# Kernel tuning notes

Measured on AMD Instinct MI355X. Metric: run time of the kernel, lower is better.

Reference implementation:

```python
import jax, jax.numpy as jnp
from jax import lax
import numpy as np

B, L, D = 2, 2048, 768
DI, DS, DTR, K = 1536, 16, 48, 4  # d_inner, d_state, dt_rank, d_conv
EPS = 1e-5


def layernorm(x, g, b):
    mu = jnp.mean(x, axis=-1, keepdims=True)
    var = jnp.mean(jnp.square(x - mu), axis=-1, keepdims=True)
    return (x - mu) * lax.rsqrt(var + EPS) * g + b


def mamba(x, in_w, conv_w, conv_b, xproj_w, dt_w, dt_b, A_log, Dp, out_w):
    # x: [B, L, D]
    xz = x @ in_w.T                       # [B, L, 2*DI]
    xc, z = jnp.split(xz, 2, axis=-1)     # [B, L, DI] each
    # causal depthwise conv1d, kernel K, left pad K-1, truncate to L
    xp = jnp.pad(xc, ((0, 0), (K - 1, 0), (0, 0)))
    conv = conv_b + sum(xp[:, k:k + L, :] * conv_w[:, k] for k in range(K))
    xc = jax.nn.silu(conv)
    dbc = xc @ xproj_w.T                  # [B, L, DTR+2*DS]
    dt = dbc[..., :DTR]
    Bm = dbc[..., DTR:DTR + DS]           # [B, L, DS]
    Cm = dbc[..., DTR + DS:]              # [B, L, DS]
    dt = jax.nn.softplus(dt @ dt_w.T + dt_b)  # [B, L, DI]
    A = -jnp.exp(A_log)                   # [DI, DS]

    def step(h, inp):
        dt_t, B_t, C_t, x_t = inp         # [B,DI], [B,DS], [B,DS], [B,DI]
        dA = jnp.exp(dt_t[..., None] * A)               # [B, DI, DS]
        h = dA * h + (dt_t * x_t)[..., None] * B_t[:, None, :]
        y = jnp.einsum('bds,bs->bd', h, C_t)
        return h, y

    h0 = jnp.zeros((x.shape[0], DI, DS), x.dtype)
    _, ys = lax.scan(step, h0, (dt.transpose(1, 0, 2), Bm.transpose(1, 0, 2),
                                Cm.transpose(1, 0, 2), xc.transpose(1, 0, 2)))
    y = ys.transpose(1, 0, 2) + xc * Dp   # [B, L, DI]
    y = y * jax.nn.silu(z)
    return y @ out_w.T                    # [B, L, D]


def setup_inputs() -> dict:
    key = jax.random.key(0)
    ks = iter(jax.random.split(key, 40))
    r = lambda s, sc=0.02: jax.random.normal(next(ks), s, jnp.float32) * sc
    A0 = jnp.log(jnp.broadcast_to(jnp.arange(1, DS + 1, dtype=jnp.float32), (DI, DS)))
    def mamba_params(p):
        return {
            f'{p}_in_w': r((2 * DI, D)), f'{p}_conv_w': r((DI, K), 0.2),
            f'{p}_conv_b': jnp.zeros((DI,)), f'{p}_xproj_w': r((DTR + 2 * DS, DI)),
            f'{p}_dt_w': r((DI, DTR), 0.1), f'{p}_dt_b': jnp.zeros((DI,)),
            f'{p}_A_log': A0, f'{p}_D': jnp.ones((DI,)), f'{p}_out_w': r((D, DI)),
        }
    inp = {'x': jax.random.normal(next(ks), (B, L, D), jnp.float32),
           'norm_g': jnp.ones((D,)), 'norm_b': jnp.zeros((D,))}
    inp.update(mamba_params('f'))
    inp.update(mamba_params('b'))
    inp.update({'mix_w': r((D, 2 * D)), 'mix_b': jnp.zeros((D,)),
                'ffn_w1': r((4 * D, D)), 'ffn_b1': jnp.zeros((4 * D,)),
                'ffn_w2': r((D, 4 * D)), 'ffn_b2': jnp.zeros((D,)),
                'ffn_norm_g': jnp.ones((D,)), 'ffn_norm_b': jnp.zeros((D,))})
    return inp


def reference(x, norm_g, norm_b,
              f_in_w, f_conv_w, f_conv_b, f_xproj_w, f_dt_w, f_dt_b, f_A_log, f_D, f_out_w,
              b_in_w, b_conv_w, b_conv_b, b_xproj_w, b_dt_w, b_dt_b, b_A_log, b_D, b_out_w,
              mix_w, mix_b, ffn_w1, ffn_b1, ffn_w2, ffn_b2, ffn_norm_g, ffn_norm_b):
    residual = x
    xn = layernorm(x, norm_g, norm_b)
    xf = mamba(xn, f_in_w, f_conv_w, f_conv_b, f_xproj_w, f_dt_w, f_dt_b, f_A_log, f_D, f_out_w)
    xb = mamba(jnp.flip(xn, axis=1), b_in_w, b_conv_w, b_conv_b, b_xproj_w,
               b_dt_w, b_dt_b, b_A_log, b_D, b_out_w)
    xb = jnp.flip(xb, axis=1)
    xm = jnp.concatenate([xf, xb], axis=-1) @ mix_w.T + mix_b
    h = xm + residual
    hn = layernorm(h, ffn_norm_g, ffn_norm_b)
    ff = jax.nn.gelu(hn @ ffn_w1.T + ffn_b1) @ ffn_w2.T + ffn_b2  # dropout = eval identity
    return ff + h
```

## Files before the change

kernel.cpp:

```cpp
#include <hip/hip_runtime.h>
#include <hip/hip_bf16.h>
#include <math.h>

#define NB 2
#define LL 2048
#define DD 768
#define DI 1536
#define DS 16
#define MM (NB*LL)
#define TCH 64
#define NCH 32

typedef __hip_bfloat16 bf16;
typedef __attribute__((ext_vector_type(8))) __bf16 bf16x8;
typedef __attribute__((ext_vector_type(4))) float f32x4;

__device__ __forceinline__ float b2f(bf16 v){ return __bfloat162float(v); }
__device__ __forceinline__ bf16 f2b(float v){ return __float2bfloat16(v); }

__device__ __forceinline__ void un2(unsigned u, float& lo, float& hi){
  union {unsigned i; float f;} a, b;
  a.i = u << 16; b.i = u & 0xffff0000u;
  lo = a.f; hi = b.f;
}

__device__ __forceinline__ void async_cp16(const bf16* g, __bf16* l) {
  __builtin_amdgcn_global_load_lds((const __attribute__((address_space(1))) void*)g,
                                   (__attribute__((address_space(3))) void*)l, 16, 0, 0);
}

#define ACT_NONE 0
#define ACT_SOFTPLUS 1
#define ACT_GELU 2

__device__ __forceinline__ float apply_act(float v, int act) {
  if (act == ACT_SOFTPLUS) {
    v = (v > 15.f) ? v : log1pf(__expf(v));
  } else if (act == ACT_GELU) {
    float u = 0.7978845608028654f * (v + 0.044715f*v*v*v);
    v = 0.5f * v * (1.f + tanhf(u));
  }
  return v;
}

__global__ void gemm_kernel(const bf16* __restrict__ A, int lda,
                            const bf16* __restrict__ B, int ldb,
                            void* __restrict__ C, int ldc,
                            int N, int K,
                            const float* __restrict__ bias,
                            const float* __restrict__ addp, int ldadd,
                            int act, int f32out)
{
  __shared__ __bf16 As[128*64];
  __shared__ __bf16 Bs[128*64];
  const int tid  = threadIdx.x;
  const int lane = tid & 63, wave = tid >> 6;
  const int m0 = blockIdx.x * 128, n0 = blockIdx.y * 128;
  const int wm = wave & 1, wn = wave >> 1;

  const int srow = wave*32 + (lane >> 3);
  const int gsw  = (lane & 7) ^ ((lane >> 3) & 7);
  const int scol = gsw * 8;
  const bf16* Ag[4]; const bf16* Bg[4];
  __bf16 *AsW[4], *BsW[4];
  #pragma unroll
  for (int i = 0; i < 4; i++) {
    int ar = m0 + srow + i*8;
    Ag[i] = A + (size_t)ar * lda + scol;
    int br = n0 + srow + i*8; if (br > N-1) br = N-1;
    Bg[i] = B + (size_t)br * ldb + scol;
    AsW[i] = &As[(wave*32 + i*8)*64];
    BsW[i] = &Bs[(wave*32 + i*8)*64];
  }

  f32x4 acc[4][4] = {};
  const int arow = wm*64 + (lane & 15);
  const int brow = wn*64 + (lane & 15);
  const int rx = lane & 7;
  const int gq = lane >> 4;

  for (int kb = 0; kb < K; kb += 64) {
    __syncthreads();
    #pragma unroll
    for (int i = 0; i < 4; i++) {
      async_cp16(Ag[i] + kb, AsW[i]);
      async_cp16(Bg[i] + kb, BsW[i]);
    }
    __syncthreads();
    #pragma unroll
    for (int h = 0; h < 2; h++) {
      const int kk = ((h*4 + gq) ^ rx) * 8;
      bf16x8 af[4], bfr[4];
      #pragma unroll
      for (int i = 0; i < 4; i++) af[i]  = *(const bf16x8*)&As[(arow + i*16)*64 + kk];
      #pragma unroll
      for (int j = 0; j < 4; j++) bfr[j] = *(const bf16x8*)&Bs[(brow + j*16)*64 + kk];
      #pragma unroll
      for (int i = 0; i < 4; i++)
        #pragma unroll
        for (int j = 0; j < 4; j++)
          acc[i][j] = __builtin_amdgcn_mfma_f32_16x16x32_bf16(af[i], bfr[j], acc[i][j], 0, 0, 0);
    }
  }

  bf16*  Cb = (bf16*)C;
  float* Cf = (float*)C;
  #pragma unroll
  for (int i = 0; i < 4; i++) {
    int rbase = m0 + wm*64 + i*16 + (lane >> 4)*4;
    #pragma unroll
    for (int j = 0; j < 4; j++) {
      int col = n0 + wn*64 + j*16 + (lane & 15);
      if (col >= N) continue;
      float bv = bias ? bias[col] : 0.f;
      #pragma unroll
      for (int r = 0; r < 4; r++) {
        int row = rbase + r;
        float v = apply_act(acc[i][j][r] + bv, act);
        if (addp) v += addp[(size_t)row * ldadd + col];
        if (f32out) Cf[(size_t)row * ldc + col] = v;
        else        Cb[(size_t)row * ldc + col] = f2b(v);
      }
    }
  }
}

__global__ void gemm64_kernel(const bf16* __restrict__ A, int lda, size_t sA,
                              const bf16* __restrict__ B, int ldb, size_t sB,
                              void* __restrict__ C, int ldc, size_t sC,
                              int N, int K,
                              const float* __restrict__ bias0,
                              const float* __restrict__ bias1, int biasBase,
                              const float* __restrict__ addp, int ldadd,
                              int act, int f32out)
{
  __shared__ __bf16 As[64*64];
  __shared__ __bf16 Bs[64*64];
  const int tid  = threadIdx.x;
  const int lane = tid & 63, wave = tid >> 6;
  const int z = blockIdx.z;
  A += (size_t)z * sA;
  B += (size_t)z * sB;
  const float* bias = ((biasBase + z) ? bias1 : bias0);
  const int m0 = blockIdx.x * 64, n0 = blockIdx.y * 64;
  const int wm = wave & 1, wn = wave >> 1;

  const int srow = wave*16 + (lane >> 3);
  const int gsw  = (lane & 7) ^ ((lane >> 3) & 7);
  const int scol = gsw * 8;
  const bf16* Ag[2]; const bf16* Bg[2];
  __bf16 *AsW[2], *BsW[2];
  #pragma unroll
  for (int i = 0; i < 2; i++) {
    int ar = m0 + srow + i*8;
    Ag[i] = A + (size_t)ar * lda + scol;
    int br = n0 + srow + i*8; if (br > N-1) br = N-1;
    Bg[i] = B + (size_t)br * ldb + scol;
    AsW[i] = &As[(wave*16 + i*8)*64];
    BsW[i] = &Bs[(wave*16 + i*8)*64];
  }

  f32x4 acc[2][2] = {};
  const int arow = wm*32 + (lane & 15);
  const int brow = wn*32 + (lane & 15);
  const int rx = lane & 7;
  const int gq = lane >> 4;

  for (int kb = 0; kb < K; kb += 64) {
    __syncthreads();
    #pragma unroll
    for (int i = 0; i < 2; i++) {
      async_cp16(Ag[i] + kb, AsW[i]);
      async_cp16(Bg[i] + kb, BsW[i]);
    }
    __syncthreads();
    #pragma unroll
    for (int h = 0; h < 2; h++) {
      const int kk = ((h*4 + gq) ^ rx) * 8;
      bf16x8 af[2], bfr[2];
      #pragma unroll
      for (int i = 0; i < 2; i++) af[i]  = *(const bf16x8*)&As[(arow + i*16)*64 + kk];
      #pragma unroll
      for (int j = 0; j < 2; j++) bfr[j] = *(const bf16x8*)&Bs[(brow + j*16)*64 + kk];
      #pragma unroll
      for (int i = 0; i < 2; i++)
        #pragma unroll
        for (int j = 0; j < 2; j++)
          acc[i][j] = __builtin_amdgcn_mfma_f32_16x16x32_bf16(af[i], bfr[j], acc[i][j], 0, 0, 0);
    }
  }

  bf16*  Cb = (bf16*)C + z*sC;
  float* Cf = (float*)C + z*sC;
  #pragma unroll
  for (int i = 0; i < 2; i++) {
    int rbase = m0 + wm*32 + i*16 + (lane >> 4)*4;
    #pragma unroll
    for (int j = 0; j < 2; j++) {
      int col = n0 + wn*32 + j*16 + (lane & 15);
      if (col >= N) continue;
      float bv = bias ? bias[col] : 0.f;
      #pragma unroll
      for (int r = 0; r < 4; r++) {
        int row = rbase + r;
        float v = apply_act(acc[i][j][r] + bv, act);
        if (addp) v += addp[(size_t)row * ldadd + col];
        if (f32out) Cf[(size_t)row * ldc + col] = v;
        else        Cb[(size_t)row * ldc + col] = f2b(v);
      }
    }
  }
}

__global__ void ln_kernel(const float* __restrict__ x, const float* __restrict__ g,
                          const float* __restrict__ b, bf16* __restrict__ out)
{
  const int row = blockIdx.x;
  const int tid = threadIdx.x;
  const float* xr = x + (size_t)row * DD;
  float v[3], s = 0.f, s2 = 0.f;
  #pragma unroll
  for (int i = 0; i < 3; i++) {
    float f = xr[tid + i*256];
    v[i] = f; s += f; s2 += f*f;
  }
  #pragma unroll
  for (int o = 32; o > 0; o >>= 1) { s += __shfl_down(s, o, 64); s2 += __shfl_down(s2, o, 64); }
  __shared__ float ps[4], ps2[4];
  int wave = tid >> 6;
  if ((tid & 63) == 0) { ps[wave] = s; ps2[wave] = s2; }
  __syncthreads();
  s = ps[0]+ps[1]+ps[2]+ps[3]; s2 = ps2[0]+ps2[1]+ps2[2]+ps2[3];
  float mu = s * (1.f/DD);
  float var = s2 * (1.f/DD) - mu*mu;
  float rs = rsqrtf(var + 1e-5f);
  #pragma unroll
  for (int i = 0; i < 3; i++) {
    int c = tid + i*256;
    float o = (v[i] - mu) * rs * g[c] + b[c];
    out[(size_t)row * DD + c] = f2b(o);
  }
}

__global__ void conv_silu_kernel(const bf16* __restrict__ xz, int ldxz, int xzDirOff,
                                 const float* __restrict__ cw0, const float* __restrict__ cb0,
                                 const float* __restrict__ cw1, const float* __restrict__ cb1,
                                 bf16* __restrict__ xc, size_t sXc, int dirBase)
{
  int idx = blockIdx.x * 256 + threadIdx.x;
  int sIdx = (idx >= DI) ? 1 : 0;
  int d = idx - sIdx*DI;
  int dir = dirBase + sIdx;
  int row = blockIdx.y;
  int b = row >> 11, t = row & 2047;
  const float* cw = dir ? cw1 : cw0;
  const float* cb = dir ? cb1 : cb0;
  float acc = cb[d];
  float w0 = cw[d*4+0], w1 = cw[d*4+1], w2 = cw[d*4+2], w3 = cw[d*4+3];
  const bf16* base = xz + (size_t)(b*2048) * ldxz + sIdx*xzDirOff + d;
  if (dir == 0) {
    if (t >= 3) acc += b2f(base[(size_t)(t-3)*ldxz]) * w0;
    if (t >= 2) acc += b2f(base[(size_t)(t-2)*ldxz]) * w1;
    if (t >= 1) acc += b2f(base[(size_t)(t-1)*ldxz]) * w2;
    acc += b2f(base[(size_t)t*ldxz]) * w3;
  } else {
    if (t <= 2044) acc += b2f(base[(size_t)(t+3)*ldxz]) * w0;
    if (t <= 2045) acc += b2f(base[(size_t)(t+2)*ldxz]) * w1;
    if (t <= 2046) acc += b2f(base[(size_t)(t+1)*ldxz]) * w2;
    acc += b2f(base[(size_t)t*ldxz]) * w3;
  }
  float y = acc / (1.f + __expf(-acc));
  xc[sIdx*sXc + (size_t)row * DI + d] = f2b(y);
}

#define SZ_INW (2*DI*DD)
#define SZ_XP  (80*DI)
#define SZ_OUT (DD*DI)
#define SZ_DTW (DI*64)
#define SZ_AN  (DI*16)
#define SZ_MIX (2*DD*DD)
#define SZ_F1  (4*DD*DD)
__global__ void prep_all_kernel(const float* fi, const float* bi,
                                const float* fxp, const float* bxp,
                                const float* fo, const float* bo,
                                const float* fdt, const float* bdt,
                                const float* fa, const float* ba,
                                const float* mw, const float* f1, const float* f2,
                                bf16* w_in, bf16* w_xp2, bf16* w_out2, bf16* dtwp2,
                                float* An2, bf16* w_mix, bf16* w_f1, bf16* w_f2)
{
  int i = blockIdx.x * 256 + threadIdx.x;
  if (i < SZ_INW) { w_in[i] = f2b(fi[i]); return; }               i -= SZ_INW;
  if (i < SZ_INW) { w_in[SZ_INW + i] = f2b(bi[i]); return; }      i -= SZ_INW;
  if (i < SZ_XP)  { w_xp2[i] = f2b(fxp[i]); return; }             i -= SZ_XP;
  if (i < SZ_XP)  { w_xp2[SZ_XP + i] = f2b(bxp[i]); return; }     i -= SZ_XP;
  if (i < SZ_OUT) { w_out2[i] = f2b(fo[i]); return; }             i -= SZ_OUT;
  if (i < SZ_OUT) { w_out2[SZ_OUT + i] = f2b(bo[i]); return; }    i -= SZ_OUT;
  if (i < SZ_DTW) { int r=i>>6,c=i&63; dtwp2[i] = (c<48)?f2b(fdt[r*48+c]):f2b(0.f); return; } i -= SZ_DTW;
  if (i < SZ_DTW) { int r=i>>6,c=i&63; dtwp2[SZ_DTW+i] = (c<48)?f2b(bdt[r*48+c]):f2b(0.f); return; } i -= SZ_DTW;
  if (i < SZ_AN)  { int d=i>>4,s=i&15; An2[s*DI+d] = -__expf(fa[i]); return; } i -= SZ_AN;
  if (i < SZ_AN)  { int d=i>>4,s=i&15; An2[SZ_AN + s*DI+d] = -__expf(ba[i]); return; } i -= SZ_AN;
  if (i < SZ_MIX) { w_mix[i] = f2b(mw[i]); return; }              i -= SZ_MIX;
  if (i < SZ_F1)  { w_f1[i] = f2b(f1[i]); return; }               i -= SZ_F1;
  w_f2[i] = f2b(f2[i]);
}

__global__ void scan_partial(const bf16* __restrict__ dt, size_t sDt,
                             const bf16* __restrict__ xc, size_t sXc,
                             const bf16* __restrict__ dbc, size_t sDbc,
                             const float* __restrict__ An, size_t sAn,
                             float* __restrict__ Pp, float* __restrict__ Sp,
                             int dirBase)
{
  const int tid = threadIdx.x;
  const int sIdx = blockIdx.z >> 1, b = blockIdx.z & 1;
  const int dir = dirBase + sIdx;
  const int c = blockIdx.y;
  const int d = blockIdx.x * 256 + tid;
  dt  += sIdx*sDt; xc += sIdx*sXc; dbc += sIdx*sDbc;
  const int rowbase = b*2048 + c*TCH;
  __shared__ unsigned bcs[TCH*16];
  for (int i = tid; i < TCH*16; i += 256) {
    int r = i >> 4, dw = i & 15;
    bcs[i] = ((const unsigned*)(dbc + (size_t)(rowbase + r)*96 + 48))[dw];
  }
  __syncthreads();
  float A[16], P[16], g[16];
  #pragma unroll
  for (int s = 0; s < 16; s++) { A[s] = An[sIdx*sAn + s*DI + d]; P[s] = 1.f; g[s] = 0.f; }
  int ph0 = dir ? (TCH-1) : 0;
  float dtv = b2f(dt[(size_t)(rowbase+ph0)*DI + d]);
  float xv  = b2f(xc[(size_t)(rowbase+ph0)*DI + d]);
  for (int t = 0; t < TCH; t++) {
    const int ph = dir ? (TCH-1-t) : t;
    const int tn = (t+1 < TCH) ? t+1 : t;
    const int phn = dir ? (TCH-1-tn) : tn;
    float dtn = b2f(dt[(size_t)(rowbase+phn)*DI + d]);
    float xvn = b2f(xc[(size_t)(rowbase+phn)*DI + d]);
    unsigned ub[8];
    *(uint4*)&ub[0] = *(const uint4*)&bcs[ph*16];
    *(uint4*)&ub[4] = *(const uint4*)&bcs[ph*16 + 4];
    float Bv[16];
    #pragma unroll
    for (int k = 0; k < 8; k++) un2(ub[k], Bv[2*k], Bv[2*k+1]);
    float u = dtv * xv;
    #pragma unroll
    for (int s = 0; s < 16; s++) {
      float dA = __expf(dtv * A[s]);
      P[s] *= dA;
      g[s] = dA * g[s] + u * Bv[s];
    }
    dtv = dtn; xv = xvn;
  }
  size_t base = ((((size_t)sIdx*NB + b)*NCH + c)*DI + d) * 16;
  #pragma unroll
  for (int s = 0; s < 16; s++) { Pp[base+s] = P[s]; Sp[base+s] = g[s]; }
}

__global__ void scan_combine(const float* __restrict__ Pp, const float* __restrict__ Sp,
                             float* __restrict__ h0, int dirBase)
{
  const int j = blockIdx.x * 256 + threadIdx.x;
  const int b = blockIdx.y;
  const int sIdx = blockIdx.z;
  const int dir = dirBase + sIdx;
  float h = 0.f;
  for (int k = 0; k < NCH; k++) {
    int c = dir ? (NCH-1-k) : k;
    size_t idx = (((size_t)sIdx*NB + b)*NCH + c)*DI*16 + j;
    h0[idx] = h;
    h = Pp[idx]*h + Sp[idx];
  }
}

__global__ void scan_final(const bf16* __restrict__ dt, size_t sDt,
                           const bf16* __restrict__ xc, size_t sXc,
                           const bf16* __restrict__ dbc, size_t sDbc,
                           const bf16* __restrict__ xz, int ldxz, int xzDirOff,
                           const float* __restrict__ An, size_t sAn,
                           const float* __restrict__ Dp0, const float* __restrict__ Dp1,
                           const float* __restrict__ h0,
                           bf16* __restrict__ yout, size_t sY, int dirBase)
{
  const int tid = threadIdx.x;
  const int sIdx = blockIdx.z >> 1, b = blockIdx.z & 1;
  const int dir = dirBase + sIdx;
  const int c = blockIdx.y;
  const int d = blockIdx.x * 256 + tid;
  dt += sIdx*sDt; xc += sIdx*sXc; dbc += sIdx*sDbc; yout += sIdx*sY;
  const float* Dp = dir ? Dp1 : Dp0;
  const int rowbase = b*2048 + c*TCH;
  __shared__ unsigned bcs[TCH*16];
  for (int i = tid; i < TCH*16; i += 256) {
    int r = i >> 4, dw = i & 15;
    bcs[i] = ((const unsigned*)(dbc + (size_t)(rowbase + r)*96 + 48))[dw];
  }
  __syncthreads();
  float A[16], h[16];
  size_t hbase = ((((size_t)sIdx*NB + b)*NCH + c)*DI + d) * 16;
  #pragma unroll
  for (int s = 0; s < 16; s++) { A[s] = An[sIdx*sAn + s*DI + d]; h[s] = h0[hbase+s]; }
  const float Dd = Dp[d];
  const bf16* zp = xz + sIdx*xzDirOff + DI + d;
  int ph0 = dir ? (TCH-1) : 0;
  float dtv = b2f(dt[(size_t)(rowbase+ph0)*DI + d]);
  float xv  = b2f(xc[(size_t)(rowbase+ph0)*DI + d]);
  float zv  = b2f(zp[(size_t)(rowbase+ph0)*ldxz]);
  for (int t = 0; t < TCH; t++) {
    const int ph = dir ? (TCH-1-t) : t;
    const int row = rowbase + ph;
    const int tn = (t+1 < TCH) ? t+1 : t;
    const int phn = dir ? (TCH-1-tn) : tn;
    float dtn = b2f(dt[(size_t)(rowbase+phn)*DI + d]);
    float xvn = b2f(xc[(size_t)(rowbase+phn)*DI + d]);
    float zvn = b2f(zp[(size_t)(rowbase+phn)*ldxz]);
    unsigned ub[8], uc[8];
    *(uint4*)&ub[0] = *(const uint4*)&bcs[ph*16];
    *(uint4*)&ub[4] = *(const uint4*)&bcs[ph*16 + 4];
    *(uint4*)&uc[0] = *(const uint4*)&bcs[ph*16 + 8];
    *(uint4*)&uc[4] = *(const uint4*)&bcs[ph*16 + 12];
    float Bv[16], Cv[16];
    #pragma unroll
    for (int k = 0; k < 8; k++) { un2(ub[k], Bv[2*k], Bv[2*k+1]); un2(uc[k], Cv[2*k], Cv[2*k+1]); }
    float u = dtv * xv;
    float y = 0.f;
    #pragma unroll
    for (int s = 0; s < 16; s++) {
      float dA = __expf(dtv * A[s]);
      h[s] = dA * h[s] + u * Bv[s];
      y += h[s] * Cv[s];
    }
    float yg = (y + xv * Dd) * (zv / (1.f + __expf(-zv)));
    yout[(size_t)row*DI + d] = f2b(yg);
    dtv = dtn; xv = xvn; zv = zvn;
  }
}

extern "C" void kernel_launch(void* const* d_in, const int* in_sizes, int n_in,
                              void* d_out, int out_size, void* d_ws, size_t ws_size,
                              hipStream_t stream)
{
  const float* x      = (const float*)d_in[0];
  const float* norm_g = (const float*)d_in[1];
  const float* norm_b = (const float*)d_in[2];
  const float* fi  = (const float*)d_in[3];
  const float* fcw = (const float*)d_in[4];
  const float* fcb = (const float*)d_in[5];
  const float* fxp = (const float*)d_in[6];
  const float* fdt = (const float*)d_in[7];
  const float* fdb = (const float*)d_in[8];
  const float* fa  = (const float*)d_in[9];
  const float* fD  = (const float*)d_in[10];
  const float* fo  = (const float*)d_in[11];
  const float* bi  = (const float*)d_in[12];
  const float* bcw = (const float*)d_in[13];
  const float* bcb = (const float*)d_in[14];
  const float* bxp = (const float*)d_in[15];
  const float* bdt = (const float*)d_in[16];
  const float* bdb = (const float*)d_in[17];
  const float* ba  = (const float*)d_in[18];
  const float* bD  = (const float*)d_in[19];
  const float* bo  = (const float*)d_in[20];
  const float* mix_w  = (const float*)d_in[21];
  const float* mix_b  = (const float*)d_in[22];
  const float* ffn_w1 = (const float*)d_in[23];
  const float* ffn_b1 = (const float*)d_in[24];
  const float* ffn_w2 = (const float*)d_in[25];
  const float* ffn_b2 = (const float*)d_in[26];
  const float* ffn_ng = (const float*)d_in[27];
  const float* ffn_nb = (const float*)d_in[28];

  auto al = [](size_t x){ return (x + 255) & ~(size_t)255; };
  const size_t fixedB =
      al((size_t)2*SZ_AN*4) + al((size_t)2*SZ_DTW*2) + al((size_t)2*SZ_INW*2) +
      al((size_t)2*SZ_XP*2) + al((size_t)2*SZ_OUT*2) + al((size_t)SZ_MIX*2) +
      al((size_t)SZ_F1*2) + al((size_t)SZ_F1*2) + al((size_t)MM*DD*2) + al((size_t)MM*DI*2);
  const size_t concB = fixedB + al((size_t)MM*2*DI*2*2) + 2*al((size_t)2*MM*DI*2) +
      al((size_t)2*MM*96*2) + 3*al((size_t)2*NB*NCH*DI*16*4);
  const bool conc = (ws_size >= concB);

  size_t o = 0;
  char* wsb = (char*)d_ws;
  auto nxt = [&](size_t bytes) -> char* {
    char* p = wsb + o; o += (bytes + 255) & ~(size_t)255; return p;
  };
  float* An2   = (float*)nxt((size_t)2*SZ_AN*4);
  bf16*  dtwp2 = (bf16*) nxt((size_t)2*SZ_DTW*2);
  bf16*  w_in  = (bf16*) nxt((size_t)2*SZ_INW*2);
  bf16*  w_xp2 = (bf16*) nxt((size_t)2*SZ_XP*2);
  bf16*  w_out2= (bf16*) nxt((size_t)2*SZ_OUT*2);
  bf16*  w_mix = (bf16*) nxt((size_t)SZ_MIX*2);
  bf16*  w_f1  = (bf16*) nxt((size_t)SZ_F1*2);
  bf16*  w_f2  = (bf16*) nxt((size_t)SZ_F1*2);
  bf16*  xn    = (bf16*) nxt((size_t)MM*DD*2);
  bf16*  xfb   = (bf16*) nxt((size_t)MM*DI*2);

  bf16 *xz, *xc, *dtb, *dbc;  float *Pp, *Sp, *h0, *hbuf;
  int ldxz, xzDirOff;
  size_t sXc, sDbc, sDt;
  if (conc) {
    xz  = (bf16*) nxt((size_t)MM*2*DI*2*2);
    xc  = (bf16*) nxt((size_t)2*MM*DI*2);
    dtb = (bf16*) nxt((size_t)2*MM*DI*2);
    dbc = (bf16*) nxt((size_t)2*MM*96*2);
    Pp  = (float*)nxt((size_t)2*NB*NCH*DI*16*4);
    Sp  = (float*)nxt((size_t)2*NB*NCH*DI*16*4);
    h0  = (float*)nxt((size_t)2*NB*NCH*DI*16*4);
    hbuf = Pp;
    ldxz = 2*2*DI; xzDirOff = 2*DI;
    sXc = (size_t)MM*DI; sDbc = (size_t)MM*96; sDt = (size_t)MM*DI;
  } else {
    xz  = (bf16*) nxt((size_t)MM*2*DI*2);
    xc  = (bf16*) nxt((size_t)MM*DI*2);
    dtb = (bf16*) nxt((size_t)MM*DI*2);
    dbc = (bf16*) nxt((size_t)MM*96*2);
    Pp  = (float*)nxt((size_t)NB*NCH*DI*16*4);
    Sp  = (float*)nxt((size_t)NB*NCH*DI*16*4);
    h0  = (float*)nxt((size_t)NB*NCH*DI*16*4);
    hbuf = (float*)dtb;
    ldxz = 2*DI; xzDirOff = 0;
    sXc = 0; sDbc = 0; sDt = 0;
  }
  bf16* hn = xn;
  bf16* a1 = xz;

  const int prepN = 2*SZ_INW + 2*SZ_XP + 2*SZ_OUT + 2*SZ_DTW + 2*SZ_AN + SZ_MIX + 2*SZ_F1;
  prep_all_kernel<<<(prepN + 255)/256, 256, 0, stream>>>(
      fi, bi, fxp, bxp, fo, bo, fdt, bdt, fa, ba, mix_w, ffn_w1, ffn_w2,
      w_in, w_xp2, w_out2, dtwp2, An2, w_mix, w_f1, w_f2);

  ln_kernel<<<MM, 256, 0, stream>>>(x, norm_g, norm_b, xn);

  if (conc) {
    gemm_kernel<<<dim3(32, 48), 256, 0, stream>>>(xn, DD, w_in, DD, xz, ldxz,
                                                  2*2*DI, DD, nullptr, nullptr, 0,
                                                  ACT_NONE, 0);
    conv_silu_kernel<<<dim3(12, MM), 256, 0, stream>>>(xz, ldxz, xzDirOff,
                                                       fcw, fcb, bcw, bcb, xc, sXc, 0);
    gemm64_kernel<<<dim3(64, 2, 2), 256, 0, stream>>>(xc, DI, sXc, w_xp2, DI, (size_t)SZ_XP,
                                                      dbc, 96, sDbc, 80, DI,
                                                      nullptr, nullptr, 0, nullptr, 0, ACT_NONE, 0);
    gemm64_kernel<<<dim3(64, 24, 2), 256, 0, stream>>>(dbc, 96, sDbc, dtwp2, 64, (size_t)SZ_DTW,
                                                       dtb, DI, sDt, DI, 64,
                                                       fdb, bdb, 0, nullptr, 0, ACT_SOFTPLUS, 0);
    scan_partial<<<dim3(DI/256, NCH, 4), 256, 0, stream>>>(dtb, sDt, xc, sXc, dbc, sDbc,
                                                           An2, (size_t)SZ_AN, Pp, Sp, 0);
    scan_combine<<<dim3(DI*16/256, NB, 2), 256, 0, stream>>>(Pp, Sp, h0, 0);
    scan_final<<<dim3(DI/256, NCH, 4), 256, 0, stream>>>(dtb, sDt, xc, sXc, dbc, sDbc,
                                                         xz, ldxz, xzDirOff, An2, (size_t)SZ_AN,
                                                         fD, bD, h0, xc, sXc, 0);
    gemm64_kernel<<<dim3(64, 12, 2), 256, 0, stream>>>(xc, DI, sXc, w_out2, DI, (size_t)SZ_OUT,
                                                       xfb, 2*DD, (size_t)DD, DD, DI,
                                                       nullptr, nullptr, 0, nullptr, 0, ACT_NONE, 0);
  } else {
    for (int dir = 0; dir < 2; ++dir) {
      gemm_kernel<<<dim3(32, 24), 256, 0, stream>>>(xn, DD, w_in + (size_t)dir*SZ_INW, DD,
                                                    xz, ldxz, 2*DI, DD, nullptr, nullptr, 0,
                                                    ACT_NONE, 0);
      conv_silu_kernel<<<dim3(6, MM), 256, 0, stream>>>(xz, ldxz, 0,
                                                        fcw, fcb, bcw, bcb, xc, 0, dir);
      gemm64_kernel<<<dim3(64, 2, 1), 256, 0, stream>>>(xc, DI, 0, w_xp2 + (size_t)dir*SZ_XP, DI, 0,
                                                        dbc, 96, 0, 80, DI,
                                                        nullptr, nullptr, 0, nullptr, 0, ACT_NONE, 0);
      gemm64_kernel<<<dim3(64, 24, 1), 256, 0, stream>>>(dbc, 96, 0, dtwp2 + (size_t)dir*SZ_DTW, 64, 0,
                                                         dtb, DI, 0, DI, 64,
                                                         fdb, bdb, dir, nullptr, 0, ACT_SOFTPLUS, 0);
      scan_partial<<<dim3(DI/256, NCH, 2), 256, 0, stream>>>(dtb, 0, xc, 0, dbc, 0,
                                                             An2 + (size_t)dir*SZ_AN, 0, Pp, Sp, dir);
      scan_combine<<<dim3(DI*16/256, NB, 1), 256, 0, stream>>>(Pp, Sp, h0, dir);
      scan_final<<<dim3(DI/256, NCH, 2), 256, 0, stream>>>(dtb, 0, xc, 0, dbc, 0,
                                                           xz, ldxz, 0, An2 + (size_t)dir*SZ_AN, 0,
                                                           fD, bD, h0, xc, 0, dir);
      gemm64_kernel<<<dim3(64, 12, 1), 256, 0, stream>>>(xc, DI, 0, w_out2 + (size_t)dir*SZ_OUT, DI, 0,
                                                         (void*)((bf16*)xfb + dir*DD), 2*DD, 0, DD, DI,
                                                         nullptr, nullptr, 0, nullptr, 0, ACT_NONE, 0);
    }
  }

  gemm64_kernel<<<dim3(64, 12, 1), 256, 0, stream>>>(xfb, 2*DD, 0, w_mix, 2*DD, 0,
                                                     hbuf, DD, 0, DD, 2*DD,
                                                     mix_b, mix_b, 0, x, DD, ACT_NONE, 1);
  ln_kernel<<<MM, 256, 0, stream>>>(hbuf, ffn_ng, ffn_nb, hn);
  gemm_kernel<<<dim3(32, 24), 256, 0, stream>>>(hn, DD, w_f1, DD, a1, 4*DD,
                                                4*DD, DD, ffn_b1, nullptr, 0, ACT_GELU, 0);
  gemm64_kernel<<<dim3(64, 12, 1), 256, 0, stream>>>(a1, 4*DD, 0, w_f2, 4*DD, 0,
                                                     d_out, DD, 0, DD, 4*DD,
                                                     ffn_b2, ffn_b2, 0, hbuf, DD, ACT_NONE, 1);
}
```

Baseline: 633.5 us.

## Add 256x256 multi-stage async GEMM and retile projection GEMMs

Adds a 512-thread GEMM with 256x256 tiles, a 4-deep async global-to-LDS pipeline using 128KB of dynamic LDS, swizzled LDS layout and raised wave priority around the MFMA loop. It is used for the in-projection and FFN-up GEMMs. The out-projection, mix and FFN-down GEMMs move from the 64-tile kernel to the 128-tile kernel, which gains batch strides. The aim is more data reuse per tile and better overlap of loads with MFMA work. The trade-off is fewer blocks than CUs for several GEMMs, so load imbalance and low occupancy are possible.

New measurement: 777.3 us. +22.7%, slower.

```diff
diff --git a/kernel.cpp b/kernel.cpp
--- a/kernel.cpp
+++ b/kernel.cpp
@@ -43,9 +43,99 @@
   return v;
 }
 
-__global__ void gemm_kernel(const bf16* __restrict__ A, int lda,
-                            const bf16* __restrict__ B, int ldb,
-                            void* __restrict__ C, int ldc,
+__global__ __launch_bounds__(512, 2)
+void gemm256_kernel(const bf16* __restrict__ A, int lda,
+                    const bf16* __restrict__ B, int ldb,
+                    bf16* __restrict__ C, int ldc, int K,
+                    const float* __restrict__ bias, int act)
+{
+  extern __shared__ __bf16 lds[];
+  __bf16* As = lds;
+  __bf16* Bs = lds + 32768;
+  const int tid  = threadIdx.x;
+  const int lane = tid & 63, wave = tid >> 6;
+  const int m0 = blockIdx.x * 256, n0 = blockIdx.y * 256;
+  const int wm = wave >> 2, wn = wave & 3;
+  const int f = lane & 15, gq = lane >> 4;
+
+  const int sl = lane >> 2, spg = lane & 3;
+  const bf16* AgS[2]; const bf16* BgS[2];
+  int dst[2];
+  #pragma unroll
+  for (int i = 0; i < 2; i++) {
+    int lr = wave*32 + i*16 + sl;
+    int lg = spg ^ (lr & 3) ^ ((lr >> 2) & 3);
+    AgS[i] = A + (size_t)(m0 + lr) * lda + lg*8;
+    BgS[i] = B + (size_t)(n0 + lr) * ldb + lg*8;
+    dst[i] = (wave*32 + i*16) * 32;
+  }
+  const int swz = (f & 3) ^ ((f >> 2) & 3);
+  const int pg8 = (gq ^ swz) * 8;
+  int aoff[8], boff[4];
+  #pragma unroll
+  for (int i = 0; i < 8; i++) aoff[i] = (wm*128 + i*16 + f)*32 + pg8;
+  #pragma unroll
+  for (int j = 0; j < 4; j++) boff[j] = (wn*64 + j*16 + f)*32 + pg8;
+
+  const int NT = K >> 5;
+#define STAGE256(tt) { \
+    const int kb_ = (tt) * 32; const int bo_ = ((tt) & 3) * 8192; \
+    async_cp16(AgS[0] + kb_, As + bo_ + dst[0]); \
+    async_cp16(AgS[1] + kb_, As + bo_ + dst[1]); \
+    async_cp16(BgS[0] + kb_, Bs + bo_ + dst[0]); \
+    async_cp16(BgS[1] + kb_, Bs + bo_ + dst[1]); }
+
+  STAGE256(0);
+  if (NT > 1) STAGE256(1);
+  if (NT > 2) STAGE256(2);
+
+  f32x4 acc[8][4] = {};
+  for (int t = 0; t < NT; ++t) {
+    asm volatile("s_waitcnt lgkmcnt(0)" ::: "memory");
+    const int ahead = NT - 1 - t;
+    if (ahead > 1)       asm volatile("s_waitcnt vmcnt(8)" ::: "memory");
+    else if (ahead == 1) asm volatile("s_waitcnt vmcnt(4)" ::: "memory");
+    else                 asm volatile("s_waitcnt vmcnt(0)" ::: "memory");
+    __builtin_amdgcn_sched_barrier(0);
+    __builtin_amdgcn_s_barrier();
+    __builtin_amdgcn_sched_barrier(0);
+    if (t + 3 < NT) STAGE256(t+3);
+    const __bf16* Ab = As + (t & 3) * 8192;
+    const __bf16* Bb = Bs + (t & 3) * 8192;
+    bf16x8 af[8], bfr[4];
+    #pragma unroll
+    for (int j = 0; j < 4; j++) bfr[j] = *(const bf16x8*)&Bb[boff[j]];
+    #pragma unroll
+    for (int i = 0; i < 8; i++) af[i] = *(const bf16x8*)&Ab[aoff[i]];
+    __builtin_amdgcn_s_setprio(1);
+    #pragma unroll
+    for (int i = 0; i < 8; i++)
+      #pragma unroll
+      for (int j = 0; j < 4; j++)
+        acc[i][j] = __builtin_amdgcn_mfma_f32_16x16x32_bf16(af[i], bfr[j], acc[i][j], 0, 0, 0);
+    __builtin_amdgcn_s_setprio(0);
+  }
+#undef STAGE256
+
+  #pragma unroll
+  for (int i = 0; i < 8; i++) {
+    const int rbase = m0 + wm*128 + i*16 + gq*4;
+    #pragma unroll
+    for (int j = 0; j < 4; j++) {
+      const int col = n0 + wn*64 + j*16 + f;
+      const float bv = bias ? bias[col] : 0.f;
+      #pragma unroll
+      for (int r = 0; r < 4; r++) {
+        float v = apply_act(acc[i][j][r] + bv, act);
+        C[(size_t)(rbase + r) * ldc + col] = f2b(v);
+      }
+    }
+  }
+}
+
+__global__ void gemm_kernel(const bf16* __restrict__ A, int lda, size_t sA,
+                            const bf16* __restrict__ B, int ldb, size_t sB,
+                            void* __restrict__ C, int ldc, size_t sC,
                             int N, int K,
                             const float* __restrict__ bias,
                             const float* __restrict__ addp, int ldadd,
@@ -55,6 +145,9 @@
   __shared__ __bf16 Bs[128*64];
   const int tid  = threadIdx.x;
   const int lane = tid & 63, wave = tid >> 6;
+  const int z = blockIdx.z;
+  A += (size_t)z * sA;
+  B += (size_t)z * sB;
   const int m0 = blockIdx.x * 128, n0 = blockIdx.y * 128;
   const int wm = wave & 1, wn = wave >> 1;
 
@@ -103,8 +196,8 @@
     }
   }
 
-  bf16*  Cb = (bf16*)C;
-  float* Cf = (float*)C;
+  bf16*  Cb = (bf16*)C + (size_t)z * sC;
+  float* Cf = (float*)C + (size_t)z * sC;
   #pragma unroll
   for (int i = 0; i < 4; i++) {
     int rbase = m0 + wm*64 + i*16 + (lane >> 4)*4;
@@ -470,6 +563,13 @@
   const float* ffn_ng = (const float*)d_in[27];
   const float* ffn_nb = (const float*)d_in[28];
 
+  static int s_attr = 0;
+  if (!s_attr) {
+    hipFuncSetAttribute((const void*)gemm256_kernel,
+                        hipFuncAttributeMaxDynamicSharedMemorySize, 131072);
+    s_attr = 1;
+  }
+
   auto al = [](size_t x){ return (x + 255) & ~(size_t)255; };
   const size_t fixedB =
       al((size_t)2*SZ_AN*4) + al((size_t)2*SZ_DTW*2) + al((size_t)2*SZ_INW*2) +
@@ -532,9 +632,8 @@
   ln_kernel<<<MM, 256, 0, stream>>>(x, norm_g, norm_b, xn);
 
   if (conc) {
-    gemm_kernel<<<dim3(32, 48), 256, 0, stream>>>(xn, DD, w_in, DD, xz, ldxz,
-                                                  2*2*DI, DD, nullptr, nullptr, 0,
-                                                  ACT_NONE, 0);
+    gemm256_kernel<<<dim3(16, 24), 512, 131072, stream>>>(xn, DD, w_in, DD,
+                                                          xz, ldxz, DD, nullptr, ACT_NONE);
     conv_silu_kernel<<<dim3(12, MM), 256, 0, stream>>>(xz, ldxz, xzDirOff,
                                                        fcw, fcb, bcw, bcb, xc, sXc, 0);
     gemm64_kernel<<<dim3(64, 2, 2), 256, 0, stream>>>(xc, DI, sXc, w_xp2, DI, (size_t)SZ_XP,
@@ -549,14 +648,13 @@
     scan_final<<<dim3(DI/256, NCH, 4), 256, 0, stream>>>(dtb, sDt, xc, sXc, dbc, sDbc,
                                                          xz, ldxz, xzDirOff, An2, (size_t)SZ_AN,
                                                          fD, bD, h0, xc, sXc, 0);
-    gemm64_kernel<<<dim3(64, 12, 2), 256, 0, stream>>>(xc, DI, sXc, w_out2, DI, (size_t)SZ_OUT,
-                                                       xfb, 2*DD, (size_t)DD, DD, DI,
-                                                       nullptr, nullptr, 0, nullptr, 0, ACT_NONE, 0);
+    gemm_kernel<<<dim3(32, 6, 2), 256, 0, stream>>>(xc, DI, sXc, w_out2, DI, (size_t)SZ_OUT,
+                                                    xfb, 2*DD, (size_t)DD, DD, DI,
+                                                    nullptr, nullptr, 0, ACT_NONE, 0);
   } else {
     for (int dir = 0; dir < 2; ++dir) {
-      gemm_kernel<<<dim3(32, 24), 256, 0, stream>>>(xn, DD, w_in + (size_t)dir*SZ_INW, DD,
-                                                    xz, ldxz, 2*DI, DD, nullptr, nullptr, 0,
-                                                    ACT_NONE, 0);
+      gemm256_kernel<<<dim3(16, 12), 512, 131072, stream>>>(xn, DD, w_in + (size_t)dir*SZ_INW, DD,
+                                                            xz, ldxz, DD, nullptr, ACT_NONE);
       conv_silu_kernel<<<dim3(6, MM), 256, 0, stream>>>(xz, ldxz, 0,
                                                         fcw, fcb, bcw, bcb, xc, 0, dir);
       gemm64_kernel<<<dim3(64, 2, 1), 256, 0, stream>>>(xc, DI, 0, w_xp2 + (size_t)dir*SZ_XP, DI, 0,
@@ -571,19 +669,19 @@
       scan_final<<<dim3(DI/256, NCH, 2), 256, 0, stream>>>(dtb, 0, xc, 0, dbc, 0,
                                                            xz, ldxz, 0, An2 + (size_t)dir*SZ_AN, 0,
                                                            fD, bD, h0, xc, 0, dir);
-      gemm64_kernel<<<dim3(64, 12, 1), 256, 0, stream>>>(xc, DI, 0, w_out2 + (size_t)dir*SZ_OUT, DI, 0,
-                                                         (void*)((bf16*)xfb + dir*DD), 2*DD, 0, DD, DI,
-                                                         nullptr, nullptr, 0, nullptr, 0, ACT_NONE, 0);
-    }
-  }
-
-  gemm64_kernel<<<dim3(64, 12, 1), 256, 0, stream>>>(xfb, 2*DD, 0, w_mix, 2*DD, 0,
-                                                     hbuf, DD, 0, DD, 2*DD,
-                                                     mix_b, mix_b, 0, x, DD, ACT_NONE, 1);
+      gemm_kernel<<<dim3(32, 6, 1), 256, 0, stream>>>(xc, DI, 0, w_out2 + (size_t)dir*SZ_OUT, DI, 0,
+                                                      (void*)((bf16*)xfb + dir*DD), 2*DD, 0, DD, DI,
+                                                      nullptr, nullptr, 0, ACT_NONE, 0);
+    }
+  }
+
+  gemm_kernel<<<dim3(32, 6, 1), 256, 0, stream>>>(xfb, 2*DD, 0, w_mix, 2*DD, 0,
+                                                  hbuf, DD, 0, DD, 2*DD,
+                                                  mix_b, x, DD, ACT_NONE, 1);
   ln_kernel<<<MM, 256, 0, stream>>>(hbuf, ffn_ng, ffn_nb, hn);
-  gemm_kernel<<<dim3(32, 24), 256, 0, stream>>>(hn, DD, w_f1, DD, a1, 4*DD,
-                                                4*DD, DD, ffn_b1, nullptr, 0, ACT_GELU, 0);
-  gemm64_kernel<<<dim3(64, 12, 1), 256, 0, stream>>>(a1, 4*DD, 0, w_f2, 4*DD, 0,
-                                                     d_out, DD, 0, DD, 4*DD,
-                                                     ffn_b2, ffn_b2, 0, hbuf, DD, ACT_NONE, 1);
-}
+  gemm256_kernel<<<dim3(16, 12), 512, 131072, stream>>>(hn, DD, w_f1, DD,
+                                                        a1, 4*DD, DD, ffn_b1, ACT_GELU);
+  gemm_kernel<<<dim3(32, 6, 1), 256, 0, stream>>>(a1, 4*DD, 0, w_f2, 4*DD, 0,
+                                                  d_out, DD, 0, DD, 4*DD,
+                                                  ffn_b2, hbuf, DD, ACT_NONE, 1);
+}
```

## Replace 128x128 GEMM with 256x256 double-buffered 8-wave ping-pong GEMM

Applied to the files above, without the earlier changes.

Replaces the single-buffered 128x128 tile GEMM with a 512-thread kernel that computes 256x256 output tiles. It uses 128KB of dynamic LDS split into double buffers, and issues async global-to-LDS copies interleaved with MFMA quarters, with explicit barriers, s_setprio and vmcnt waits. The aim is to overlap global loads with matrix math and raise data reuse per tile for the in-projection and FFN-up GEMMs. It drops the N-bounds clamping and the residual-add/f32 output paths, so it relies on N and K being multiples of 256 and 128. The larger tile also gives fewer blocks: 384 for the in-projection and 192 for FFN-up.

Measured after the change: 677.3 us. 6.9% more time.

```diff
diff --git a/kernel.cpp b/kernel.cpp
--- a/kernel.cpp
+++ b/kernel.cpp
@@ -43,86 +43,123 @@
   return v;
 }
 
-__global__ void gemm_kernel(const bf16* __restrict__ A, int lda,
-                            const bf16* __restrict__ B, int ldb,
-                            void* __restrict__ C, int ldc,
-                            int N, int K,
-                            const float* __restrict__ bias,
-                            const float* __restrict__ addp, int ldadd,
-                            int act, int f32out)
-{
-  __shared__ __bf16 As[128*64];
-  __shared__ __bf16 Bs[128*64];
+__global__ __launch_bounds__(512, 2)
+void gemm8p_kernel(const bf16* __restrict__ A, int lda,
+                   const bf16* __restrict__ B, int ldb,
+                   bf16* __restrict__ C, int ldc, int K,
+                   const float* __restrict__ bias, int act)
+{
+  extern __shared__ __bf16 lds[];
+  __bf16* As = lds;
+  __bf16* Bs = lds + 32768;
   const int tid  = threadIdx.x;
   const int lane = tid & 63, wave = tid >> 6;
-  const int m0 = blockIdx.x * 128, n0 = blockIdx.y * 128;
-  const int wm = wave & 1, wn = wave >> 1;
-
-  const int srow = wave*32 + (lane >> 3);
-  const int gsw  = (lane & 7) ^ ((lane >> 3) & 7);
-  const int scol = gsw * 8;
-  const bf16* Ag[4]; const bf16* Bg[4];
-  __bf16 *AsW[4], *BsW[4];
-  #pragma unroll
-  for (int i = 0; i < 4; i++) {
-    int ar = m0 + srow + i*8;
-    Ag[i] = A + (size_t)ar * lda + scol;
-    int br = n0 + srow + i*8; if (br > N-1) br = N-1;
-    Bg[i] = B + (size_t)br * ldb + scol;
-    AsW[i] = &As[(wave*32 + i*8)*64];
-    BsW[i] = &Bs[(wave*32 + i*8)*64];
-  }
-
-  f32x4 acc[4][4] = {};
-  const int arow = wm*64 + (lane & 15);
-  const int brow = wn*64 + (lane & 15);
-  const int rx = lane & 7;
-  const int gq = lane >> 4;
-
-  for (int kb = 0; kb < K; kb += 64) {
-    __syncthreads();
+  const int m0 = blockIdx.x * 256, n0 = blockIdx.y * 256;
+  const int wm = wave >> 2, wn = wave & 3;
+  const int f = lane & 15, gq = lane >> 4, rx = lane & 7;
+
+  const int srow = wave*16 + (lane >> 3);
+  const int sgrp = (lane & 7) ^ ((lane >> 3) & 7);
+  const bf16* Ast = A + (size_t)(m0 + srow) * lda + sgrp*8;
+  const bf16* Bst = B + (size_t)(n0 + srow) * ldb + sgrp*8;
+  const size_t lda8 = (size_t)8*lda, ldb8 = (size_t)8*ldb;
+  const size_t lda128 = (size_t)128*lda, ldb128 = (size_t)128*ldb;
+  const int sdst = wave*16*64;
+
+#define STG_A(buf, half, kt) { \
+    async_cp16(Ast + (half)*lda128 + (kt)*64,        As + (buf)*16384 + (half)*8192 + sdst); \
+    async_cp16(Ast + (half)*lda128 + lda8 + (kt)*64, As + (buf)*16384 + (half)*8192 + sdst + 512); }
+#define STG_B(buf, half, kt) { \
+    async_cp16(Bst + (half)*ldb128 + (kt)*64,        Bs + (buf)*16384 + (half)*8192 + sdst); \
+    async_cp16(Bst + (half)*ldb128 + ldb8 + (kt)*64, Bs + (buf)*16384 + (half)*8192 + sdst + 512); }
+
+  const int kk0 = (gq ^ rx) * 8;
+  const int kk1 = ((4 + gq) ^ rx) * 8;
+  const int arow = (wm*128 + f) * 64;
+  const int brow = (wn*64  + f) * 64;
+  bf16x8 af[4][2], b0[2][2], b1[2][2];
+
+#define RD_A(buf, mq) { _Pragma("unroll") for (int i = 0; i < 4; i++) { \
+    const __bf16* p = &As[(buf)*16384 + arow + ((mq)*64 + i*16)*64]; \
+    af[i][0] = *(const bf16x8*)&p[kk0]; af[i][1] = *(const bf16x8*)&p[kk1]; } }
+#define RD_B(buf, nq, dst) { _Pragma("unroll") for (int j = 0; j < 2; j++) { \
+    const __bf16* p = &Bs[(buf)*16384 + brow + ((nq)*32 + j*16)*64]; \
+    dst[j][0] = *(const bf16x8*)&p[kk0]; dst[j][1] = *(const bf16x8*)&p[kk1]; } }
+#define MFQ(mq, nq, bset) { __builtin_amdgcn_s_setprio(1); \
+    _Pragma("unroll") for (int i = 0; i < 4; i++) \
+      _Pragma("unroll") for (int j = 0; j < 2; j++) { \
+        acc[(mq)*4+i][(nq)*2+j] = __builtin_amdgcn_mfma_f32_16x16x32_bf16(af[i][0], bset[j][0], acc[(mq)*4+i][(nq)*2+j], 0,0,0); \
+        acc[(mq)*4+i][(nq)*2+j] = __builtin_amdgcn_mfma_f32_16x16x32_bf16(af[i][1], bset[j][1], acc[(mq)*4+i][(nq)*2+j], 0,0,0); } \
+    __builtin_amdgcn_s_setprio(0); }
+#define SBAR { __builtin_amdgcn_sched_barrier(0); __builtin_amdgcn_s_barrier(); __builtin_amdgcn_sched_barrier(0); }
+
+  f32x4 acc[8][4] = {};
+  const int NT = K >> 6, NT2 = K >> 7;
+
+  STG_A(0,0,0); STG_A(0,1,0); STG_B(0,0,0); STG_B(0,1,0);
+  STG_B(1,0,1); STG_B(1,1,1);
+  asm volatile("s_waitcnt vmcnt(4)" ::: "memory");
+  SBAR;
+
+  for (int it = 0; it < NT2; ++it) {
+    const int te = 2*it, to = te + 1;
+    const bool more  = (te + 2 < NT);
+    const bool more3 = (to + 2 < NT);
+    const bool lastit = (it == NT2 - 1);
+    RD_A(0,0); RD_B(0,0,b0);
+    STG_A(1,0,to);
+    SBAR; MFQ(0,0,b0); SBAR;
+    RD_B(0,1,b1);
+    STG_A(1,1,to);
+    SBAR; MFQ(0,1,b1); SBAR;
+    RD_A(0,1);
+    if (more) STG_B(0,0,te+2);
+    SBAR; MFQ(1,0,b0); SBAR;
+    if (more) STG_B(0,1,te+2);
+    SBAR; MFQ(1,1,b1);
+    if (lastit) { asm volatile("s_waitcnt vmcnt(0)" ::: "memory"); }
+    else        { asm volatile("s_waitcnt vmcnt(4)" ::: "memory"); }
+    SBAR;
+    RD_A(1,0); RD_B(1,0,b0);
+    if (more) STG_A(0,0,te+2);
+    SBAR; MFQ(0,0,b0); SBAR;
+    RD_B(1,1,b1);
+    if (more) STG_A(0,1,te+2);
+    SBAR; MFQ(0,1,b1); SBAR;
+    RD_A(1,1);
+    if (more3) STG_B(1,0,to+2);
+    SBAR; MFQ(1,0,b0); SBAR;
+    if (more3) STG_B(1,1,to+2);
+    SBAR; MFQ(1,1,b1);
+    if (lastit) { asm volatile("s_waitcnt vmcnt(0)" ::: "memory"); }
+    else        { asm volatile("s_waitcnt vmcnt(4)" ::: "memory"); }
+    SBAR;
+  }
+#undef STG_A
+#undef STG_B
+#undef RD_A
+#undef RD_B
+#undef MFQ
+#undef SBAR
+
+  #pragma unroll
+  for (int mq = 0; mq < 2; mq++)
     #pragma unroll
     for (int i = 0; i < 4; i++) {
-      async_cp16(Ag[i] + kb, AsW[i]);
-      async_cp16(Bg[i] + kb, BsW[i]);
+      const int rbase = m0 + wm*128 + mq*64 + i*16 + gq*4;
+      #pragma unroll
+      for (int nq = 0; nq < 2; nq++)
+        #pragma unroll
+        for (int j = 0; j < 2; j++) {
+          const int col = n0 + wn*64 + nq*32 + j*16 + f;
+          const float bv = bias ? bias[col] : 0.f;
+          #pragma unroll
+          for (int r = 0; r < 4; r++) {
+            float v = apply_act(acc[mq*4+i][nq*2+j][r] + bv, act);
+            C[(size_t)(rbase + r) * ldc + col] = f2b(v);
+          }
+        }
     }
-    __syncthreads();
-    #pragma unroll
-    for (int h = 0; h < 2; h++) {
-      const int kk = ((h*4 + gq) ^ rx) * 8;
-      bf16x8 af[4], bfr[4];
-      #pragma unroll
-      for (int i = 0; i < 4; i++) af[i]  = *(const bf16x8*)&As[(arow + i*16)*64 + kk];
-      #pragma unroll
-      for (int j = 0; j < 4; j++) bfr[j] = *(const bf16x8*)&Bs[(brow + j*16)*64 + kk];
-      #pragma unroll
-      for (int i = 0; i < 4; i++)
-        #pragma unroll
-        for (int j = 0; j < 4; j++)
-          acc[i][j] = __builtin_amdgcn_mfma_f32_16x16x32_bf16(af[i], bfr[j], acc[i][j], 0, 0, 0);
-    }
-  }
-
-  bf16*  Cb = (bf16*)C;
-  float* Cf = (float*)C;
-  #pragma unroll
-  for (int i = 0; i < 4; i++) {
-    int rbase = m0 + wm*64 + i*16 + (lane >> 4)*4;
-    #pragma unroll
-    for (int j = 0; j < 4; j++) {
-      int col = n0 + wn*64 + j*16 + (lane & 15);
-      if (col >= N) continue;
-      float bv = bias ? bias[col] : 0.f;
-      #pragma unroll
-      for (int r = 0; r < 4; r++) {
-        int row = rbase + r;
-        float v = apply_act(acc[i][j][r] + bv, act);
-        if (addp) v += addp[(size_t)row * ldadd + col];
-        if (f32out) Cf[(size_t)row * ldc + col] = v;
-        else        Cb[(size_t)row * ldc + col] = f2b(v);
-      }
-    }
-  }
 }
 
 __global__ void gemm64_kernel(const bf16* __restrict__ A, int lda, size_t sA,
@@ -470,6 +507,13 @@
   const float* ffn_ng = (const float*)d_in[27];
   const float* ffn_nb = (const float*)d_in[28];
 
+  static int s_attr = 0;
+  if (!s_attr) {
+    hipFuncSetAttribute((const void*)gemm8p_kernel,
+                        hipFuncAttributeMaxDynamicSharedMemorySize, 131072);
+    s_attr = 1;
+  }
+
   auto al = [](size_t x){ return (x + 255) & ~(size_t)255; };
   const size_t fixedB =
       al((size_t)2*SZ_AN*4) + al((size_t)2*SZ_DTW*2) + al((size_t)2*SZ_INW*2) +
@@ -532,9 +576,8 @@
   ln_kernel<<<MM, 256, 0, stream>>>(x, norm_g, norm_b, xn);
 
   if (conc) {
-    gemm_kernel<<<dim3(32, 48), 256, 0, stream>>>(xn, DD, w_in, DD, xz, ldxz,
-                                                  2*2*DI, DD, nullptr, nullptr, 0,
-                                                  ACT_NONE, 0);
+    gemm8p_kernel<<<dim3(16, 24), 512, 131072, stream>>>(xn, DD, w_in, DD,
+                                                         xz, ldxz, DD, nullptr, ACT_NONE);
     conv_silu_kernel<<<dim3(12, MM), 256, 0, stream>>>(xz, ldxz, xzDirOff,
                                                        fcw, fcb, bcw, bcb, xc, sXc, 0);
     gemm64_kernel<<<dim3(64, 2, 2), 256, 0, stream>>>(xc, DI, sXc, w_xp2, DI, (size_t)SZ_XP,
@@ -554,9 +597,8 @@
                                                        nullptr, nullptr, 0, nullptr, 0, ACT_NONE, 0);
   } else {
     for (int dir = 0; dir < 2; ++dir) {
-      gemm_kernel<<<dim3(32, 24), 256, 0, stream>>>(xn, DD, w_in + (size_t)dir*SZ_INW, DD,
-                                                    xz, ldxz, 2*DI, DD, nullptr, nullptr, 0,
-                                                    ACT_NONE, 0);
+      gemm8p_kernel<<<dim3(16, 12), 512, 131072, stream>>>(xn, DD, w_in + (size_t)dir*SZ_INW, DD,
+                                                           xz, ldxz, DD, nullptr, ACT_NONE);
       conv_silu_kernel<<<dim3(6, MM), 256, 0, stream>>>(xz, ldxz, 0,
                                                         fcw, fcb, bcw, bcb, xc, 0, dir);
       gemm64_kernel<<<dim3(64, 2, 1), 256, 0, stream>>>(xc, DI, 0, w_xp2 + (size_t)dir*SZ_XP, DI, 0,
@@ -581,8 +623,8 @@
                                                      hbuf, DD, 0, DD, 2*DD,
                                                      mix_b, mix_b, 0, x, DD, ACT_NONE, 1);
   ln_kernel<<<MM, 256, 0, stream>>>(hbuf, ffn_ng, ffn_nb, hn);
-  gemm_kernel<<<dim3(32, 24), 256, 0, stream>>>(hn, DD, w_f1, DD, a1, 4*DD,
-                                                4*DD, DD, ffn_b1, nullptr, 0, ACT_GELU, 0);
+  gemm8p_kernel<<<dim3(16, 12), 512, 131072, stream>>>(hn, DD, w_f1, DD,
+                                                       a1, 4*DD, DD, ffn_b1, ACT_GELU);
   gemm64_kernel<<<dim3(64, 12, 1), 256, 0, stream>>>(a1, 4*DD, 0, w_f2, 4*DD, 0,
                                                      d_out, DD, 0, DD, 4*DD,
                                                      ffn_b2, ffn_b2, 0, hbuf, DD, ACT_NONE, 1);
```

## Double-buffer shared-memory tiles in both GEMM kernels to overlap loads with MFMA

Applied to the files above, without the earlier changes.

Both GEMM kernels now keep two LDS buffers for the A and B tiles. Each iteration issues the async copies for the next K-tile before running the MFMAs on the current one, and the loop uses one barrier per iteration instead of two. The aim is to hide global-to-LDS latency behind compute, at the cost of twice the LDS per block, which may lower occupancy. It relies on the async copies finishing before the barrier at the end of the iteration.

Measured after the change: 696.8 us. +10.0%, slower.

```diff
diff --git a/kernel.cpp b/kernel.cpp
--- a/kernel.cpp
+++ b/kernel.cpp
@@ -51,8 +51,8 @@
                             const float* __restrict__ addp, int ldadd,
                             int act, int f32out)
 {
-  __shared__ __bf16 As[128*64];
-  __shared__ __bf16 Bs[128*64];
+  __shared__ __bf16 As[2][128*64];
+  __shared__ __bf16 Bs[2][128*64];
   const int tid  = threadIdx.x;
   const int lane = tid & 63, wave = tid >> 6;
   const int m0 = blockIdx.x * 128, n0 = blockIdx.y * 128;
@@ -62,16 +62,19 @@
   const int gsw  = (lane & 7) ^ ((lane >> 3) & 7);
   const int scol = gsw * 8;
   const bf16* Ag[4]; const bf16* Bg[4];
-  __bf16 *AsW[4], *BsW[4];
+  int ldst[4];
   #pragma unroll
   for (int i = 0; i < 4; i++) {
     int ar = m0 + srow + i*8;
     Ag[i] = A + (size_t)ar * lda + scol;
     int br = n0 + srow + i*8; if (br > N-1) br = N-1;
     Bg[i] = B + (size_t)br * ldb + scol;
-    AsW[i] = &As[(wave*32 + i*8)*64];
-    BsW[i] = &Bs[(wave*32 + i*8)*64];
-  }
+    ldst[i] = (wave*32 + i*8)*64;
+  }
+
+#define STG128(buf, kb) { _Pragma("unroll") for (int i = 0; i < 4; i++) { \
+    async_cp16(Ag[i] + (kb), &As[buf][ldst[i]]); \
+    async_cp16(Bg[i] + (kb), &Bs[buf][ldst[i]]); } }
 
   f32x4 acc[4][4] = {};
   const int arow = wm*64 + (lane & 15);
@@ -79,29 +82,31 @@
   const int rx = lane & 7;
   const int gq = lane >> 4;
 
+  STG128(0, 0);
+  __syncthreads();
+  int cur = 0;
   for (int kb = 0; kb < K; kb += 64) {
-    __syncthreads();
-    #pragma unroll
-    for (int i = 0; i < 4; i++) {
-      async_cp16(Ag[i] + kb, AsW[i]);
-      async_cp16(Bg[i] + kb, BsW[i]);
-    }
-    __syncthreads();
+    if (kb + 64 < K) STG128(cur^1, kb+64);
+    const __bf16* Asc = As[cur];
+    const __bf16* Bsc = Bs[cur];
     #pragma unroll
     for (int h = 0; h < 2; h++) {
       const int kk = ((h*4 + gq) ^ rx) * 8;
       bf16x8 af[4], bfr[4];
       #pragma unroll
-      for (int i = 0; i < 4; i++) af[i]  = *(const bf16x8*)&As[(arow + i*16)*64 + kk];
-      #pragma unroll
-      for (int j = 0; j < 4; j++) bfr[j] = *(const bf16x8*)&Bs[(brow + j*16)*64 + kk];
+      for (int i = 0; i < 4; i++) af[i]  = *(const bf16x8*)&Asc[(arow + i*16)*64 + kk];
+      #pragma unroll
+      for (int j = 0; j < 4; j++) bfr[j] = *(const bf16x8*)&Bsc[(brow + j*16)*64 + kk];
       #pragma unroll
       for (int i = 0; i < 4; i++)
         #pragma unroll
         for (int j = 0; j < 4; j++)
           acc[i][j] = __builtin_amdgcn_mfma_f32_16x16x32_bf16(af[i], bfr[j], acc[i][j], 0, 0, 0);
     }
-  }
+    __syncthreads();
+    cur ^= 1;
+  }
+#undef STG128
 
   bf16*  Cb = (bf16*)C;
   float* Cf = (float*)C;
@@ -134,8 +139,8 @@
                               const float* __restrict__ addp, int ldadd,
                               int act, int f32out)
 {
-  __shared__ __bf16 As[64*64];
-  __shared__ __bf16 Bs[64*64];
+  __shared__ __bf16 As[2][64*64];
+  __shared__ __bf16 Bs[2][64*64];
   const int tid  = threadIdx.x;
   const int lane = tid & 63, wave = tid >> 6;
   const int z = blockIdx.z;
@@ -149,16 +154,19 @@
   const int gsw  = (lane & 7) ^ ((lane >> 3) & 7);
   const int scol = gsw * 8;
   const bf16* Ag[2]; const bf16* Bg[2];
-  __bf16 *AsW[2], *BsW[2];
+  int ldst[2];
   #pragma unroll
   for (int i = 0; i < 2; i++) {
     int ar = m0 + srow + i*8;
     Ag[i] = A + (size_t)ar * lda + scol;
     int br = n0 + srow + i*8; if (br > N-1) br = N-1;
     Bg[i] = B + (size_t)br * ldb + scol;
-    AsW[i] = &As[(wave*16 + i*8)*64];
-    BsW[i] = &Bs[(wave*16 + i*8)*64];
-  }
+    ldst[i] = (wave*16 + i*8)*64;
+  }
+
+#define STG64(buf, kb) { _Pragma("unroll") for (int i = 0; i < 2; i++) { \
+    async_cp16(Ag[i] + (kb), &As[buf][ldst[i]]); \
+    async_cp16(Bg[i] + (kb), &Bs[buf][ldst[i]]); } }
 
   f32x4 acc[2][2] = {};
   const int arow = wm*32 + (lane & 15);
@@ -166,29 +174,31 @@
   const int rx = lane & 7;
   const int gq = lane >> 4;
 
+  STG64(0, 0);
+  __syncthreads();
+  int cur = 0;
   for (int kb = 0; kb < K; kb += 64) {
-    __syncthreads();
-    #pragma unroll
-    for (int i = 0; i < 2; i++) {
-      async_cp16(Ag[i] + kb, AsW[i]);
-      async_cp16(Bg[i] + kb, BsW[i]);
-    }
-    __syncthreads();
+    if (kb + 64 < K) STG64(cur^1, kb+64);
+    const __bf16* Asc = As[cur];
+    const __bf16* Bsc = Bs[cur];
     #pragma unroll
     for (int h = 0; h < 2; h++) {
       const int kk = ((h*4 + gq) ^ rx) * 8;
       bf16x8 af[2], bfr[2];
       #pragma unroll
-      for (int i = 0; i < 2; i++) af[i]  = *(const bf16x8*)&As[(arow + i*16)*64 + kk];
-      #pragma unroll
-      for (int j = 0; j < 2; j++) bfr[j] = *(const bf16x8*)&Bs[(brow + j*16)*64 + kk];
+      for (int i = 0; i < 2; i++) af[i]  = *(const bf16x8*)&Asc[(arow + i*16)*64 + kk];
+      #pragma unroll
+      for (int j = 0; j < 2; j++) bfr[j] = *(const bf16x8*)&Bsc[(brow + j*16)*64 + kk];
       #pragma unroll
       for (int i = 0; i < 2; i++)
         #pragma unroll
         for (int j = 0; j < 2; j++)
           acc[i][j] = __builtin_amdgcn_mfma_f32_16x16x32_bf16(af[i], bfr[j], acc[i][j], 0, 0, 0);
     }
-  }
+    __syncthreads();
+    cur ^= 1;
+  }
+#undef STG64
 
   bf16*  Cb = (bf16*)C + z*sC;
   float* Cf = (float*)C + z*sC;
```
